# Performance work log

Measured on AMD Instinct MI355X. Metric: run time of the kernel, lower is better.

Reference implementation:

```python
import jax, jax.numpy as jnp
import numpy as np

B, L, D = 2, 2048, 1024
H, DK, DV = 16, 64, 64
EPS = 1e-6


def setup_inputs() -> dict:
    key = jax.random.key(0)
    ks = jax.random.split(key, 7)
    s = 0.02
    return {
        "x": jax.random.normal(ks[0], (B, L, D), dtype=jnp.float32),
        "Wq": jax.random.normal(ks[1], (D, H * DK), dtype=jnp.float32) * s,
        "Wk": jax.random.normal(ks[2], (D, H * DK), dtype=jnp.float32) * s,
        "Wv": jax.random.normal(ks[3], (D, H * DV), dtype=jnp.float32) * s,
        "Wo": jax.random.normal(ks[4], (H * DV, D), dtype=jnp.float32) * s,
        "ln_gamma": jnp.ones((D,), dtype=jnp.float32),
        "ln_beta": jnp.zeros((D,), dtype=jnp.float32),
    }


def reference(x, Wq, Wk, Wv, Wo, ln_gamma, ln_beta):
    temp = jnp.asarray(DK, x.dtype) ** 0.5
    # projections -> [B, H, L, Dh]
    q = (x @ Wq).reshape(B, L, H, DK).transpose(0, 2, 1, 3)
    k = (x @ Wk).reshape(B, L, H, DK).transpose(0, 2, 1, 3)
    v = (x @ Wv).reshape(B, L, H, DV).transpose(0, 2, 1, 3)
    # naive attention: explicit [B,H,L,L] scores (dropout rate 0 -> identity)
    scores = jnp.einsum("bhqd,bhkd->bhqk", q / temp, k)
    attn = jax.nn.softmax(scores, axis=-1)
    o = jnp.einsum("bhqk,bhkd->bhqd", attn, v)
    o = o.transpose(0, 2, 1, 3).reshape(B, L, H * DV)
    out = o @ Wo + x  # residual
    # LayerNorm(eps=1e-6)
    mu = jnp.mean(out, axis=-1, keepdims=True)
    var = jnp.var(out, axis=-1, keepdims=True)
    return (out - mu) * jax.lax.rsqrt(var + EPS) * ln_gamma + ln_beta
```

## Files before the change

### kernel.cpp

```cpp
#include <hip/hip_runtime.h>


typedef __bf16 bf16;
typedef __bf16 bf16x2 __attribute__((ext_vector_type(2)));
typedef __bf16 bf16x4 __attribute__((ext_vector_type(4)));
typedef __bf16 bf16x8 __attribute__((ext_vector_type(8)));
typedef float floatx4 __attribute__((ext_vector_type(4)));
typedef int intx4 __attribute__((ext_vector_type(4)));

#define MFMA16(a, b, c) __builtin_amdgcn_mfma_f32_16x16x32_bf16((a), (b), (c), 0, 0, 0)

__device__ __forceinline__ void gll16(const bf16* g, bf16* l) {
  __builtin_amdgcn_global_load_lds((const __attribute__((address_space(1))) void*)g,
                                   (__attribute__((address_space(3))) void*)l, 16, 0, 0);
}

__global__ __launch_bounds__(256) void k_prep_x(const float* __restrict__ x, bf16* __restrict__ xb) {
  const int i = (blockIdx.x * 256 + threadIdx.x) * 4;
  const float4 v = *reinterpret_cast<const float4*>(x + i);
  bf16x4 o = {(bf16)v.x, (bf16)v.y, (bf16)v.z, (bf16)v.w};
  *reinterpret_cast<bf16x4*>(xb + i) = o;
}

__global__ __launch_bounds__(256) void k_prep_w(const float* __restrict__ Wq, const float* __restrict__ Wk,
                                                const float* __restrict__ Wv, const float* __restrict__ Wo,
                                                bf16* __restrict__ WT) {
  __shared__ float tile[32][33];
  const int z = blockIdx.z;
  const float* W = (z == 0) ? Wq : (z == 1) ? Wk : (z == 2) ? Wv : Wo;
  const int n0 = blockIdx.x * 32, k0 = blockIdx.y * 32;
  const int tx = threadIdx.x, ty = threadIdx.y;
#pragma unroll
  for (int j = 0; j < 32; j += 8)
    tile[ty + j][tx] = W[(size_t)(k0 + ty + j) * 1024 + n0 + tx];
  __syncthreads();
#pragma unroll
  for (int j = 0; j < 32; j += 8)
    WT[(size_t)(z * 1024 + n0 + ty + j) * 1024 + k0 + tx] = (bf16)tile[tx][ty + j];
}

template <int MODE>
__global__ __launch_bounds__(256) void k_gemm(const bf16* __restrict__ A, const bf16* __restrict__ Bt,
                                              const float* __restrict__ X, float* __restrict__ Y,
                                              bf16* __restrict__ QB, bf16* __restrict__ KB,
                                              bf16* __restrict__ VTB) {
  __shared__ __align__(16) bf16 As[128 * 64];
  __shared__ __align__(16) bf16 Bs[128 * 64];
  const int t = threadIdx.x;
  const int lane = t & 63, wv = t >> 6;
  const int qd = lane >> 4, col = lane & 15;
  const int c7 = col & 7;
  const int wm = wv >> 1, wn = wv & 1;
  const int m0 = blockIdx.x * 128, n0 = blockIdx.y * 128;
  const int srow = wv * 8 + (lane >> 3);
  const int scol = ((lane & 7) ^ (lane >> 3)) * 8;
  const bf16* Ag = A + (size_t)(m0 + srow) * 1024 + scol;
  const bf16* Bg = Bt + (size_t)(n0 + srow) * 1024 + scol;

  floatx4 acc[4][4] = {};

  for (int kt = 0; kt < 1024; kt += 64) {
    __syncthreads();
#pragma unroll
    for (int rd = 0; rd < 4; rd++) {
      gll16(Ag + (size_t)rd * 32 * 1024 + kt, As + (rd * 32 + wv * 8) * 64);
      gll16(Bg + (size_t)rd * 32 * 1024 + kt, Bs + (rd * 32 + wv * 8) * 64);
    }
    __syncthreads();
#pragma unroll
    for (int ks = 0; ks < 2; ks++) {
      bf16x8 af[4], bfr[4];
#pragma unroll
      for (int i = 0; i < 4; i++)
        af[i] = *reinterpret_cast<const bf16x8*>(As + (wm * 64 + i * 16 + col) * 64 + ((ks * 4 + qd) ^ c7) * 8);
#pragma unroll
      for (int i = 0; i < 4; i++)
        bfr[i] = *reinterpret_cast<const bf16x8*>(Bs + (wn * 64 + i * 16 + col) * 64 + ((ks * 4 + qd) ^ c7) * 8);
#pragma unroll
      for (int i = 0; i < 4; i++)
#pragma unroll
        for (int j = 0; j < 4; j++)
          acc[i][j] = MFMA16(af[i], bfr[j], acc[i][j]);
    }
  }

#pragma unroll
  for (int i = 0; i < 4; i++) {
#pragma unroll
    for (int j = 0; j < 4; j++) {
      const int mb = m0 + wm * 64 + i * 16 + qd * 4;
      const int n = n0 + wn * 64 + j * 16 + col;
      if (MODE == 0) {
        const int seg = n >> 10;
        const int h = (n & 1023) >> 6, dd = n & 63;
#pragma unroll
        for (int r = 0; r < 4; r++) {
          const int m = mb + r;
          const int bb = m >> 11, l = m & 2047;
          const float v = acc[i][j][r];
          if (seg == 0)
            QB[((size_t)(bb * 16 + h) * 2048 + l) * 64 + dd] = (bf16)(v * 0.125f);
          else if (seg == 1)
            KB[((size_t)(bb * 16 + h) * 2048 + l) * 64 + dd] = (bf16)v;
          else
            VTB[((size_t)(bb * 16 + h) * 64 + dd) * 2048 + l] = (bf16)v;
        }
      } else {
#pragma unroll
        for (int r = 0; r < 4; r++) {
          const int m = mb + r;
          Y[(size_t)m * 1024 + n] = acc[i][j][r] + X[(size_t)m * 1024 + n];
        }
      }
    }
  }
}

__global__ __launch_bounds__(256) void k_attn(const bf16* __restrict__ QB, const bf16* __restrict__ KB,
                                              const bf16* __restrict__ VTB, bf16* __restrict__ OB) {
  __shared__ __align__(16) bf16 Ks[2][64 * 64];
  __shared__ __align__(16) bf16 Vs[2][64 * 64];
  const int t = threadIdx.x;
  const int lane = t & 63, wv = t >> 6;
  const int qd = lane >> 4, col = lane & 15;
  const int c7 = col & 7;
  const int bh = blockIdx.y;
  const int qr = blockIdx.x * 128 + wv * 32;
  const int lrow0 = wv * 8 + (lane >> 3);
  const int scol = ((lane & 7) ^ (lane >> 3)) * 8;
  const int kg0 = ((lrow0 >> 5) << 5) + (((lrow0 >> 2) & 3) << 3) + (((lrow0 >> 4) & 1) << 2) + (lrow0 & 3);
  const int r1 = lrow0 + 32;
  const int kg1 = ((r1 >> 5) << 5) + (((r1 >> 2) & 3) << 3) + (((r1 >> 4) & 1) << 2) + (r1 & 3);
  const bf16* Kg0 = KB + ((size_t)bh * 2048 + kg0) * 64 + scol;
  const bf16* Kg1 = KB + ((size_t)bh * 2048 + kg1) * 64 + scol;
  const bf16* Vg0 = VTB + ((size_t)bh * 64 + lrow0) * 2048 + scol;
  const bf16* Vg1 = VTB + ((size_t)bh * 64 + lrow0 + 32) * 2048 + scol;

  bf16x8 bQ[2][2];
#pragma unroll
  for (int qt = 0; qt < 2; qt++)
#pragma unroll
    for (int s = 0; s < 2; s++)
      bQ[qt][s] = *reinterpret_cast<const bf16x8*>(QB + ((size_t)bh * 2048 + qr + qt * 16 + col) * 64 + s * 32 + qd * 8);

  floatx4 oacc[2][4] = {};
  float lsum[2] = {0.f, 0.f};
  floatx4 scur[2][4];
  int pk[2][4][2];

#define STAGE(i)                                                      \
  do {                                                                \
    const int b_ = (i) & 1;                                           \
    gll16(Kg0 + (size_t)(i) * 4096, &Ks[b_][(wv * 8) * 64]);          \
    gll16(Kg1 + (size_t)(i) * 4096, &Ks[b_][(32 + wv * 8) * 64]);     \
    gll16(Vg0 + (i) * 64, &Vs[b_][(wv * 8) * 64]);                    \
    gll16(Vg1 + (i) * 64, &Vs[b_][(32 + wv * 8) * 64]);               \
  } while (0)

#define QK(i)                                                                                       \
  do {                                                                                              \
    const bf16* ks_ = Ks[(i) & 1];                                                                  \
    _Pragma("unroll") for (int nt = 0; nt < 4; nt++) {                                              \
      bf16x8 a0 = *reinterpret_cast<const bf16x8*>(ks_ + (nt * 16 + col) * 64 + (qd ^ c7) * 8);     \
      bf16x8 a1 = *reinterpret_cast<const bf16x8*>(ks_ + (nt * 16 + col) * 64 + ((4 + qd) ^ c7) * 8); \
      _Pragma("unroll") for (int qt = 0; qt < 2; qt++) {                                            \
        floatx4 z = {0.f, 0.f, 0.f, 0.f};                                                           \
        z = MFMA16(a0, bQ[qt][0], z);                                                               \
        z = MFMA16(a1, bQ[qt][1], z);                                                               \
        scur[qt][nt] = z;                                                                           \
      }                                                                                             \
    }                                                                                               \
  } while (0)

#define EXPPACK()                                                                               \
  do {                                                                                          \
    _Pragma("unroll") for (int qt = 0; qt < 2; qt++) {                                          \
      _Pragma("unroll") for (int nt = 0; nt < 4; nt++) {                                        \
        const float e0 = __expf(scur[qt][nt][0]), e1 = __expf(scur[qt][nt][1]);                 \
        const float e2 = __expf(scur[qt][nt][2]), e3 = __expf(scur[qt][nt][3]);                 \
        lsum[qt] += (e0 + e1) + (e2 + e3);                                                      \
        bf16x2 p01, p23;                                                                        \
        p01[0] = (bf16)e0; p01[1] = (bf16)e1;                                                   \
        p23[0] = (bf16)e2; p23[1] = (bf16)e3;                                                   \
        pk[qt][nt][0] = __builtin_bit_cast(int, p01);                                           \
        pk[qt][nt][1] = __builtin_bit_cast(int, p23);                                           \
      }                                                                                         \
    }                                                                                           \
  } while (0)

#define PV(i)                                                                                       \
  do {                                                                                              \
    const bf16* vs_ = Vs[(i) & 1];                                                                  \
    bf16x8 bV[4][2];                                                                                \
    _Pragma("unroll") for (int nd = 0; nd < 4; nd++) {                                              \
      bV[nd][0] = *reinterpret_cast<const bf16x8*>(vs_ + (nd * 16 + col) * 64 + (qd ^ c7) * 8);     \
      bV[nd][1] = *reinterpret_cast<const bf16x8*>(vs_ + (nd * 16 + col) * 64 + ((4 + qd) ^ c7) * 8); \
    }                                                                                               \
    _Pragma("unroll") for (int qt = 0; qt < 2; qt++) {                                              \
      _Pragma("unroll") for (int s = 0; s < 2; s++) {                                               \
        intx4 w;                                                                                    \
        w[0] = pk[qt][2 * s][0]; w[1] = pk[qt][2 * s][1];                                           \
        w[2] = pk[qt][2 * s + 1][0]; w[3] = pk[qt][2 * s + 1][1];                                   \
        const bf16x8 aP = __builtin_bit_cast(bf16x8, w);                                            \
        _Pragma("unroll") for (int nd = 0; nd < 4; nd++)                                            \
          oacc[qt][nd] = MFMA16(aP, bV[nd][s], oacc[qt][nd]);                                       \
      }                                                                                             \
    }                                                                                               \
  } while (0)

  STAGE(0);
  __syncthreads();
  QK(0);
  for (int i = 1; i < 32; i++) {
    __syncthreads();
    STAGE(i);
    EXPPACK();
    PV(i - 1);
    __syncthreads();
    QK(i);
  }
  EXPPACK();
  PV(31);

#pragma unroll
  for (int qt = 0; qt < 2; qt++) {
    lsum[qt] += __shfl_xor(lsum[qt], 16);
    lsum[qt] += __shfl_xor(lsum[qt], 32);
  }
  const int bb = bh >> 4, h = bh & 15;
#pragma unroll
  for (int qt = 0; qt < 2; qt++) {
#pragma unroll
    for (int r = 0; r < 4; r++) {
      const float linv = 1.f / __shfl(lsum[qt], qd * 4 + r);
      const size_t m = (size_t)bb * 2048 + qr + qt * 16 + qd * 4 + r;
#pragma unroll
      for (int nd = 0; nd < 4; nd++)
        OB[m * 1024 + h * 64 + nd * 16 + col] = (bf16)(oacc[qt][nd][r] * linv);
    }
  }
#undef STAGE
#undef QK
#undef EXPPACK
#undef PV
}

__global__ __launch_bounds__(256) void k_ln(const float* __restrict__ Yin, const float* __restrict__ gamma,
                                            const float* __restrict__ beta, float* __restrict__ out) {
  __shared__ float red[8];
  const int row = blockIdx.x, t = threadIdx.x;
  const float4 v = *reinterpret_cast<const float4*>(Yin + (size_t)row * 1024 + t * 4);
  float s = v.x + v.y + v.z + v.w;
  float ss = v.x * v.x + v.y * v.y + v.z * v.z + v.w * v.w;
#pragma unroll
  for (int d = 1; d < 64; d <<= 1) {
    s += __shfl_xor(s, d);
    ss += __shfl_xor(ss, d);
  }
  if ((t & 63) == 0) {
    red[t >> 6] = s;
    red[4 + (t >> 6)] = ss;
  }
  __syncthreads();
  s = red[0] + red[1] + red[2] + red[3];
  ss = red[4] + red[5] + red[6] + red[7];
  const float mu = s * (1.f / 1024.f);
  const float var = ss * (1.f / 1024.f) - mu * mu;
  const float rs = rsqrtf(var + 1e-6f);
  const float4 g = *reinterpret_cast<const float4*>(gamma + t * 4);
  const float4 bt = *reinterpret_cast<const float4*>(beta + t * 4);
  float4 o;
  o.x = (v.x - mu) * rs * g.x + bt.x;
  o.y = (v.y - mu) * rs * g.y + bt.y;
  o.z = (v.z - mu) * rs * g.z + bt.z;
  o.w = (v.w - mu) * rs * g.w + bt.w;
  *reinterpret_cast<float4*>(out + (size_t)row * 1024 + t * 4) = o;
}

extern "C" void kernel_launch(void* const* d_in, const int* in_sizes, int n_in,
                              void* d_out, int out_size, void* d_ws, size_t ws_size,
                              hipStream_t stream) {
  (void)in_sizes; (void)n_in; (void)out_size; (void)ws_size;
  const float* x = (const float*)d_in[0];
  const float* Wq = (const float*)d_in[1];
  const float* Wk = (const float*)d_in[2];
  const float* Wv = (const float*)d_in[3];
  const float* Wo = (const float*)d_in[4];
  const float* gamma = (const float*)d_in[5];
  const float* beta = (const float*)d_in[6];

  char* ws = (char*)d_ws;
  const size_t MB = 1ull << 20;
  bf16* XB = (bf16*)(ws);
  bf16* OB = (bf16*)(ws);
  bf16* WT = (bf16*)(ws + 8 * MB);
  bf16* QB = (bf16*)(ws + 16 * MB);
  bf16* KB = (bf16*)(ws + 24 * MB);
  bf16* VTB = (bf16*)(ws + 32 * MB);
  float* Y = (float*)(ws + 16 * MB);

  k_prep_x<<<4096, 256, 0, stream>>>(x, XB);
  k_prep_w<<<dim3(32, 32, 4), dim3(32, 8), 0, stream>>>(Wq, Wk, Wv, Wo, WT);
  k_gemm<0><<<dim3(32, 24), 256, 0, stream>>>(XB, WT, nullptr, nullptr, QB, KB, VTB);
  k_attn<<<dim3(16, 32), 256, 0, stream>>>(QB, KB, VTB, OB);
  k_gemm<1><<<dim3(32, 8), 256, 0, stream>>>(OB, WT + (size_t)3072 * 1024, x, Y,
                                             nullptr, nullptr, nullptr);
  k_ln<<<4096, 256, 0, stream>>>(Y, gamma, beta, (float*)d_out);
}
```

Before: 208.1 us.

## Double-buffer LDS tiles in projection GEMM to overlap loads with MFMA

Doubles the shared-memory A/B tiles and prefetches the next K-tile with global_load_lds while the current tile feeds the MFMAs. This hides the global-load latency that the single-buffer loop exposed between syncs. It costs twice the LDS per block (64KB), which may lower occupancy, and it adds explicit vmcnt waits.

```diff
diff --git a/kernel.cpp b/kernel.cpp
--- a/kernel.cpp
+++ b/kernel.cpp
@@ -44,8 +44,8 @@
                                               const float* __restrict__ X, float* __restrict__ Y,
                                               bf16* __restrict__ QB, bf16* __restrict__ KB,
                                               bf16* __restrict__ VTB) {
-  __shared__ __align__(16) bf16 As[128 * 64];
-  __shared__ __align__(16) bf16 Bs[128 * 64];
+  __shared__ __align__(16) bf16 As[2 * 128 * 64];
+  __shared__ __align__(16) bf16 Bs[2 * 128 * 64];
   const int t = threadIdx.x;
   const int lane = t & 63, wv = t >> 6;
   const int qd = lane >> 4, col = lane & 15;
@@ -59,30 +59,48 @@
 
   floatx4 acc[4][4] = {};
 
-  for (int kt = 0; kt < 1024; kt += 64) {
+#define GSTAGE(ktv, buf)                                                                            \
+  do {                                                                                              \
+    _Pragma("unroll") for (int rd = 0; rd < 4; rd++) {                                              \
+      gll16(Ag + (size_t)rd * 32 * 1024 + (ktv), As + (buf) * 8192 + (rd * 32 + wv * 8) * 64);      \
+      gll16(Bg + (size_t)rd * 32 * 1024 + (ktv), Bs + (buf) * 8192 + (rd * 32 + wv * 8) * 64);      \
+    }                                                                                               \
+  } while (0)
+
+#define GCOMP(buf)                                                                                  \
+  do {                                                                                              \
+    const bf16* as_ = As + (buf) * 8192;                                                            \
+    const bf16* bs_ = Bs + (buf) * 8192;                                                            \
+    _Pragma("unroll") for (int ks = 0; ks < 2; ks++) {                                              \
+      bf16x8 af[4], bfr[4];                                                                         \
+      _Pragma("unroll") for (int i = 0; i < 4; i++)                                                 \
+        af[i] = *reinterpret_cast<const bf16x8*>(as_ + (wm * 64 + i * 16 + col) * 64 +              \
+                                                 ((ks * 4 + qd) ^ c7) * 8);                         \
+      _Pragma("unroll") for (int i = 0; i < 4; i++)                                                 \
+        bfr[i] = *reinterpret_cast<const bf16x8*>(bs_ + (wn * 64 + i * 16 + col) * 64 +             \
+                                                  ((ks * 4 + qd) ^ c7) * 8);                        \
+      _Pragma("unroll") for (int i = 0; i < 4; i++)                                                 \
+        _Pragma("unroll") for (int j = 0; j < 4; j++)                                               \
+          acc[i][j] = MFMA16(af[i], bfr[j], acc[i][j]);                                             \
+    }                                                                                               \
+  } while (0)
+
+  GSTAGE(0, 0);
+  asm volatile("s_waitcnt vmcnt(0)" ::: "memory");
+  __syncthreads();
+
+  for (int kt = 0; kt < 1024; kt += 128) {
+    GSTAGE(kt + 64, 1);
+    GCOMP(0);
+    asm volatile("s_waitcnt vmcnt(0)" ::: "memory");
     __syncthreads();
-#pragma unroll
-    for (int rd = 0; rd < 4; rd++) {
-      gll16(Ag + (size_t)rd * 32 * 1024 + kt, As + (rd * 32 + wv * 8) * 64);
-      gll16(Bg + (size_t)rd * 32 * 1024 + kt, Bs + (rd * 32 + wv * 8) * 64);
-    }
+    if (kt + 128 < 1024) GSTAGE(kt + 128, 0);
+    GCOMP(1);
+    asm volatile("s_waitcnt vmcnt(0)" ::: "memory");
     __syncthreads();
-#pragma unroll
-    for (int ks = 0; ks < 2; ks++) {
-      bf16x8 af[4], bfr[4];
-#pragma unroll
-      for (int i = 0; i < 4; i++)
-        af[i] = *reinterpret_cast<const bf16x8*>(As + (wm * 64 + i * 16 + col) * 64 + ((ks * 4 + qd) ^ c7) * 8);
-#pragma unroll
-      for (int i = 0; i < 4; i++)
-        bfr[i] = *reinterpret_cast<const bf16x8*>(Bs + (wn * 64 + i * 16 + col) * 64 + ((ks * 4 + qd) ^ c7) * 8);
-#pragma unroll
-      for (int i = 0; i < 4; i++)
-#pragma unroll
-        for (int j = 0; j < 4; j++)
-          acc[i][j] = MFMA16(af[i], bfr[j], acc[i][j]);
-    }
-  }
+  }
+#undef GSTAGE
+#undef GCOMP
 
 #pragma unroll
   for (int i = 0; i < 4; i++) {
```

Measured after the change: 216.8 us. 1.04x slower.
